# Kernel tuning notes

Hardware: AMD Instinct MI355X
Metric: run time of the kernel (lower is better)

Reference implementation:

```python
import jax, jax.numpy as jnp
import numpy as np

KS = 11  # conv kernel size, padding = KS//2 -> SAME


def setup_inputs() -> dict:
    key = jax.random.key(0)
    ks = jax.random.split(key, 6)
    B, H, W = 16, 256, 256
    x = jax.random.uniform(ks[0], (B, 1, H, W), jnp.float32)
    # conv_same(1,1,ks=11,bias=False) -> OIHW kernel [1,1,11,11]
    K = jax.random.normal(ks[1], (1, 1, KS, KS), jnp.float32) * (1.0 / KS)
    # rule: Linear(1,10) -> ReLU -> Linear(10,10) -> ReLU -> Linear(10,1), all with bias
    w1 = jax.random.normal(ks[2], (10, 1), jnp.float32) * 0.5
    b1 = jnp.zeros((10,), jnp.float32)
    w2 = jax.random.normal(ks[3], (10, 10), jnp.float32) * 0.3
    b2 = jnp.zeros((10,), jnp.float32)
    w3 = jax.random.normal(ks[4], (1, 10), jnp.float32) * 0.3
    b3 = jnp.zeros((1,), jnp.float32)
    return {"x": x, "K": K, "w1": w1, "b1": b1, "w2": w2, "b2": b2,
            "w3": w3, "b3": b3, "steps": 16}


def reference(x, K, w1, b1, w2, b2, w3, b3, steps):
    # One NCA step: 11x11 single-channel conv -> pointwise 3-layer MLP on the
    # channel dim (Permute makes Linear act per-pixel) -> clipped residual add.
    def step(xc, _):
        out = jax.lax.conv_general_dilated(
            xc, K, window_strides=(1, 1), padding="SAME",
            dimension_numbers=("NCHW", "OIHW", "NCHW"))  # [B,1,H,W]
        v = out[:, 0]                                   # [B,H,W]
        h = jax.nn.relu(v[..., None] * w1[:, 0] + b1)   # [B,H,W,10]
        h = jax.nn.relu(jnp.einsum("bhwi,oi->bhwo", h, w2) + b2)
        y = jnp.einsum("bhwi,oi->bhwo", h, w3) + b3     # [B,H,W,1]
        xn = jnp.clip(xc + jnp.moveaxis(y, -1, 1), 0.0, 1.0)
        return xn, xn

    _, seq = jax.lax.scan(step, x, None, length=steps)
    # torch returns a list [x0, x1, ..., x_steps]; we stack it.
    return jnp.concatenate([x[None], seq], axis=0)  # [steps+1, B, 1, H, W]
```

## Files before the change

### kernel.cpp

```cpp
#include <hip/hip_runtime.h>


#define HH 256
#define WW 256
#define BB 16
#define TH 16
#define TW 64
#define SH (TH + 10)
#define SW (TW + 10)
#define SWP 76
#define SLAB (BB * HH * WW)

__global__ __launch_bounds__(256) void nca_copy_x(const float* __restrict__ x,
                                                  float* __restrict__ out) {
    int i = (blockIdx.x * 256 + threadIdx.x) * 4;
    *(float4*)(out + i) = *(const float4*)(x + i);
}

__global__ __launch_bounds__(256) void nca_step(
    const float* __restrict__ src, float* __restrict__ dst,
    const float* __restrict__ Kk,
    const float* __restrict__ w1, const float* __restrict__ b1,
    const float* __restrict__ w2, const float* __restrict__ b2,
    const float* __restrict__ w3, const float* __restrict__ b3) {
    __shared__ __align__(16) float s[SH * SWP];

    const int tid = threadIdx.x;
    const int b   = blockIdx.z;
    const int gy0 = blockIdx.y * TH;
    const int gx0 = blockIdx.x * TW;
    const float* img = src + b * HH * WW;

    for (int i = tid; i < SH * SW; i += 256) {
        int r = i / SW, c = i - r * SW;
        int gy = gy0 - 5 + r, gx = gx0 - 5 + c;
        float v = 0.f;
        if (gy >= 0 && gy < HH && gx >= 0 && gx < WW) v = img[gy * WW + gx];
        s[r * SWP + c] = v;
    }
    __syncthreads();

    const int tx = tid & 15, ty = tid >> 4;
    const int x0 = tx * 4;

    float acc0 = 0.f, acc1 = 0.f, acc2 = 0.f, acc3 = 0.f;
#pragma unroll
    for (int ky = 0; ky < 11; ++ky) {
        const float* row = &s[(ty + ky) * SWP + x0];
        float win[16];
        *(float4*)(win + 0)  = *(const float4*)(row + 0);
        *(float4*)(win + 4)  = *(const float4*)(row + 4);
        *(float4*)(win + 8)  = *(const float4*)(row + 8);
        *(float2*)(win + 12) = *(const float2*)(row + 12);
#pragma unroll
        for (int kx = 0; kx < 11; ++kx) {
            float kv = Kk[ky * 11 + kx];
            acc0 = fmaf(win[kx + 0], kv, acc0);
            acc1 = fmaf(win[kx + 1], kv, acc1);
            acc2 = fmaf(win[kx + 2], kv, acc2);
            acc3 = fmaf(win[kx + 3], kv, acc3);
        }
    }

    const float b3v = b3[0];
    float vacc[4] = {acc0, acc1, acc2, acc3};
    float res[4];
#pragma unroll
    for (int p = 0; p < 4; ++p) {
        float v = vacc[p];
        float h1[10];
#pragma unroll
        for (int i = 0; i < 10; ++i)
            h1[i] = fmaxf(fmaf(v, w1[i], b1[i]), 0.f);
        float y = b3v;
#pragma unroll
        for (int o = 0; o < 10; ++o) {
            float a = b2[o];
#pragma unroll
            for (int i = 0; i < 10; ++i)
                a = fmaf(h1[i], w2[o * 10 + i], a);
            y = fmaf(fmaxf(a, 0.f), w3[o], y);
        }
        float xc = s[(ty + 5) * SWP + x0 + 5 + p];
        res[p] = fminf(fmaxf(xc + y, 0.f), 1.f);
    }

    float* orow = dst + b * HH * WW + (gy0 + ty) * WW + gx0 + x0;
    *(float4*)orow = make_float4(res[0], res[1], res[2], res[3]);
}

extern "C" void kernel_launch(void* const* d_in, const int* in_sizes, int n_in,
                              void* d_out, int out_size, void* d_ws, size_t ws_size,
                              hipStream_t stream) {
    const float* x  = (const float*)d_in[0];
    const float* Kk = (const float*)d_in[1];
    const float* w1 = (const float*)d_in[2];
    const float* b1 = (const float*)d_in[3];
    const float* w2 = (const float*)d_in[4];
    const float* b2 = (const float*)d_in[5];
    const float* w3 = (const float*)d_in[6];
    const float* b3 = (const float*)d_in[7];
    float* out = (float*)d_out;

    nca_copy_x<<<SLAB / (256 * 4), 256, 0, stream>>>(x, out);

    dim3 grid(WW / TW, HH / TH, BB);
    for (int k = 0; k < 16; ++k) {
        nca_step<<<grid, 256, 0, stream>>>(out + (size_t)k * SLAB,
                                           out + (size_t)(k + 1) * SLAB,
                                           Kk, w1, b1, w2, b2, w3, b3);
    }
}
```

Measured before the change: 288.4 us.

## Fuse all NCA steps into one persistent kernel with grid barriers

Replaces the copy kernel plus 16 per-step launches with a single persistent kernel of 1024 blocks that synchronises between steps through an atomic-counter grid barrier. The x0 copy is folded into the first step. Separately, when all b1 entries are zero, the first two MLP layers collapse into a per-sign linear map (relu(v*w1) = v*max(w1,0) for v>=0), so each pixel needs 10 FMAs for the hidden layer instead of about 110. The barrier depends on all 1024 blocks being co-resident, which is checked only through the occupancy query with no cooperative-launch guarantee. The fast MLP path relies on the test's zero biases but keeps a general fallback.

```diff
diff --git a/kernel.cpp b/kernel.cpp
--- a/kernel.cpp
+++ b/kernel.cpp
@@ -10,27 +10,51 @@
 #define SW (TW + 10)
 #define SWP 76
 #define SLAB (BB * HH * WW)
-
-__global__ __launch_bounds__(256) void nca_copy_x(const float* __restrict__ x,
-                                                  float* __restrict__ out) {
-    int i = (blockIdx.x * 256 + threadIdx.x) * 4;
-    *(float4*)(out + i) = *(const float4*)(x + i);
-}
-
-__global__ __launch_bounds__(256) void nca_step(
-    const float* __restrict__ src, float* __restrict__ dst,
+#define NSTEPS 16
+#define NB 1024
+
+__device__ __forceinline__ void grid_bar(unsigned* cnt, unsigned target) {
+    __syncthreads();
+    if (threadIdx.x == 0) {
+        __threadfence();
+        __hip_atomic_fetch_add(cnt, 1u, __ATOMIC_RELAXED, __HIP_MEMORY_SCOPE_AGENT);
+        while (__hip_atomic_load(cnt, __ATOMIC_RELAXED, __HIP_MEMORY_SCOPE_AGENT) < target)
+            __builtin_amdgcn_s_sleep(1);
+        __threadfence();
+    }
+    __syncthreads();
+}
+
+__device__ __forceinline__ void mlp_precompute(
+    const float* __restrict__ w1, const float* __restrict__ b1,
+    const float* __restrict__ w2, bool& fast, float (&cp)[10], float (&cn)[10]) {
+    fast = true;
+#pragma unroll
+    for (int i = 0; i < 10; ++i) fast = fast && (b1[i] == 0.f);
+#pragma unroll
+    for (int o = 0; o < 10; ++o) { cp[o] = 0.f; cn[o] = 0.f; }
+    if (fast) {
+#pragma unroll
+        for (int i = 0; i < 10; ++i) {
+            float wi = w1[i];
+            float p = fmaxf(wi, 0.f), n = fminf(wi, 0.f);
+#pragma unroll
+            for (int o = 0; o < 10; ++o) {
+                cp[o] = fmaf(p, w2[o * 10 + i], cp[o]);
+                cn[o] = fmaf(n, w2[o * 10 + i], cn[o]);
+            }
+        }
+    }
+}
+
+__device__ __forceinline__ void step_tile(
+    const float* __restrict__ img, float* __restrict__ dst, float* __restrict__ t0,
+    float* s, int gy0, int gx0, int tid, bool fast,
+    const float (&cp)[10], const float (&cn)[10],
     const float* __restrict__ Kk,
     const float* __restrict__ w1, const float* __restrict__ b1,
     const float* __restrict__ w2, const float* __restrict__ b2,
-    const float* __restrict__ w3, const float* __restrict__ b3) {
-    __shared__ __align__(16) float s[SH * SWP];
-
-    const int tid = threadIdx.x;
-    const int b   = blockIdx.z;
-    const int gy0 = blockIdx.y * TH;
-    const int gx0 = blockIdx.x * TW;
-    const float* img = src + b * HH * WW;
-
+    const float* __restrict__ w3, float b3v) {
     for (int i = tid; i < SH * SW; i += 256) {
         int r = i / SW, c = i - r * SW;
         int gy = gy0 - 5 + r, gx = gx0 - 5 + c;
@@ -62,31 +86,103 @@
         }
     }
 
-    const float b3v = b3[0];
     float vacc[4] = {acc0, acc1, acc2, acc3};
     float res[4];
-#pragma unroll
-    for (int p = 0; p < 4; ++p) {
-        float v = vacc[p];
-        float h1[10];
-#pragma unroll
-        for (int i = 0; i < 10; ++i)
-            h1[i] = fmaxf(fmaf(v, w1[i], b1[i]), 0.f);
-        float y = b3v;
-#pragma unroll
-        for (int o = 0; o < 10; ++o) {
-            float a = b2[o];
+    if (fast) {
+#pragma unroll
+        for (int p = 0; p < 4; ++p) {
+            float v = vacc[p];
+            bool pos = (v >= 0.f);
+            float y = b3v;
+#pragma unroll
+            for (int o = 0; o < 10; ++o) {
+                float c = pos ? cp[o] : cn[o];
+                float a = fmaf(v, c, b2[o]);
+                y = fmaf(fmaxf(a, 0.f), w3[o], y);
+            }
+            float xc = s[(ty + 5) * SWP + x0 + 5 + p];
+            res[p] = fminf(fmaxf(xc + y, 0.f), 1.f);
+        }
+    } else {
+#pragma unroll
+        for (int p = 0; p < 4; ++p) {
+            float v = vacc[p];
+            float h1[10];
 #pragma unroll
             for (int i = 0; i < 10; ++i)
-                a = fmaf(h1[i], w2[o * 10 + i], a);
-            y = fmaf(fmaxf(a, 0.f), w3[o], y);
-        }
-        float xc = s[(ty + 5) * SWP + x0 + 5 + p];
-        res[p] = fminf(fmaxf(xc + y, 0.f), 1.f);
-    }
-
-    float* orow = dst + b * HH * WW + (gy0 + ty) * WW + gx0 + x0;
+                h1[i] = fmaxf(fmaf(v, w1[i], b1[i]), 0.f);
+            float y = b3v;
+#pragma unroll
+            for (int o = 0; o < 10; ++o) {
+                float a = b2[o];
+#pragma unroll
+                for (int i = 0; i < 10; ++i)
+                    a = fmaf(h1[i], w2[o * 10 + i], a);
+                y = fmaf(fmaxf(a, 0.f), w3[o], y);
+            }
+            float xc = s[(ty + 5) * SWP + x0 + 5 + p];
+            res[p] = fminf(fmaxf(xc + y, 0.f), 1.f);
+        }
+    }
+
+    if (t0) {
+        const float* c0 = &s[(ty + 5) * SWP + x0 + 5];
+        float* o0 = t0 + (gy0 + ty) * WW + gx0 + x0;
+        *(float4*)o0 = make_float4(c0[0], c0[1], c0[2], c0[3]);
+    }
+    float* orow = dst + (gy0 + ty) * WW + gx0 + x0;
     *(float4*)orow = make_float4(res[0], res[1], res[2], res[3]);
+}
+
+__global__ __launch_bounds__(256, 4) void nca_persist(
+    const float* __restrict__ x, float* __restrict__ out, unsigned* cnt,
+    const float* __restrict__ Kk,
+    const float* __restrict__ w1, const float* __restrict__ b1,
+    const float* __restrict__ w2, const float* __restrict__ b2,
+    const float* __restrict__ w3, const float* __restrict__ b3) {
+    __shared__ __align__(16) float s[SH * SWP];
+    const int tid = threadIdx.x;
+    const int bid = blockIdx.x;
+    const int gx0 = (bid & 3) * TW;
+    const int gy0 = ((bid >> 2) & 15) * TH;
+    const int b   = bid >> 6;
+    const float b3v = b3[0];
+
+    bool fast; float cp[10], cn[10];
+    mlp_precompute(w1, b1, w2, fast, cp, cn);
+
+    for (int k = 0; k < NSTEPS; ++k) {
+        if (k > 0) grid_bar(cnt, (unsigned)(NB * k));
+        const float* img = (k == 0 ? x : out + (size_t)k * SLAB) + b * HH * WW;
+        float* dst = out + (size_t)(k + 1) * SLAB + b * HH * WW;
+        float* t0  = (k == 0) ? out + b * HH * WW : nullptr;
+        step_tile(img, dst, t0, s, gy0, gx0, tid, fast, cp, cn,
+                  Kk, w1, b1, w2, b2, w3, b3v);
+    }
+}
+
+__global__ __launch_bounds__(256) void nca_copy_x(const float* __restrict__ x,
+                                                  float* __restrict__ out) {
+    int i = (blockIdx.x * 256 + threadIdx.x) * 4;
+    *(float4*)(out + i) = *(const float4*)(x + i);
+}
+
+__global__ __launch_bounds__(256) void nca_step(
+    const float* __restrict__ src, float* __restrict__ dst,
+    const float* __restrict__ Kk,
+    const float* __restrict__ w1, const float* __restrict__ b1,
+    const float* __restrict__ w2, const float* __restrict__ b2,
+    const float* __restrict__ w3, const float* __restrict__ b3) {
+    __shared__ __align__(16) float s[SH * SWP];
+    const int tid = threadIdx.x;
+    const int b   = blockIdx.z;
+    const int gy0 = blockIdx.y * TH;
+    const int gx0 = blockIdx.x * TW;
+    const float b3v = b3[0];
+    bool fast; float cp[10], cn[10];
+    mlp_precompute(w1, b1, w2, fast, cp, cn);
+    step_tile(src + b * HH * WW, dst + b * HH * WW, nullptr, s, gy0, gx0, tid,
+              fast, cp, cn, Kk, w1, b1, w2, b2, w3, b3v);
 }
 
 extern "C" void kernel_launch(void* const* d_in, const int* in_sizes, int n_in,
@@ -102,12 +198,24 @@
     const float* b3 = (const float*)d_in[7];
     float* out = (float*)d_out;
 
-    nca_copy_x<<<SLAB / (256 * 4), 256, 0, stream>>>(x, out);
-
-    dim3 grid(WW / TW, HH / TH, BB);
-    for (int k = 0; k < 16; ++k) {
-        nca_step<<<grid, 256, 0, stream>>>(out + (size_t)k * SLAB,
-                                           out + (size_t)(k + 1) * SLAB,
-                                           Kk, w1, b1, w2, b2, w3, b3);
-    }
-}
+    static int maxb = -1;
+    if (maxb < 0) {
+        if (hipOccupancyMaxActiveBlocksPerMultiprocessor(
+                &maxb, (const void*)nca_persist, 256, 0) != hipSuccess)
+            maxb = 0;
+    }
+
+    if (maxb >= 4 && d_ws != nullptr && ws_size >= 64) {
+        hipMemsetAsync(d_ws, 0, 64, stream);
+        nca_persist<<<NB, 256, 0, stream>>>(x, out, (unsigned*)d_ws,
+                                            Kk, w1, b1, w2, b2, w3, b3);
+    } else {
+        nca_copy_x<<<SLAB / (256 * 4), 256, 0, stream>>>(x, out);
+        dim3 grid(WW / TW, HH / TH, BB);
+        for (int k = 0; k < 16; ++k) {
+            nca_step<<<grid, 256, 0, stream>>>(out + (size_t)k * SLAB,
+                                               out + (size_t)(k + 1) * SLAB,
+                                               Kk, w1, b1, w2, b2, w3, b3);
+        }
+    }
+}
```

Result: slower. 360.1 us (+24.8%).

## Collapse zero-bias MLP into sign-split linear form and fuse initial copy

Applied to the files above, without the earlier changes.

When the first-layer biases are all zero, relu(v*w1) is piecewise linear in v, so the first two layers fold into two precomputed 10-vectors chosen by the sign of v. This cuts the per-pixel MLP cost from about 110 FMAs to about 20. The separate kernel that copies x into output slot 0 is removed, and the first step writes that slab from its shared-memory tile. Each thread redoes a small per-block precompute, and a general fallback path remains for nonzero biases.

```diff
diff --git a/kernel.cpp b/kernel.cpp
--- a/kernel.cpp
+++ b/kernel.cpp
@@ -11,14 +11,60 @@
 #define SWP 76
 #define SLAB (BB * HH * WW)
 
-__global__ __launch_bounds__(256) void nca_copy_x(const float* __restrict__ x,
-                                                  float* __restrict__ out) {
-    int i = (blockIdx.x * 256 + threadIdx.x) * 4;
-    *(float4*)(out + i) = *(const float4*)(x + i);
+__device__ __forceinline__ void mlp_precompute(
+    const float* __restrict__ w1, const float* __restrict__ b1,
+    const float* __restrict__ w2, bool& fast, float (&cp)[10], float (&cn)[10]) {
+    fast = true;
+#pragma unroll
+    for (int i = 0; i < 10; ++i) fast = fast && (b1[i] == 0.f);
+#pragma unroll
+    for (int o = 0; o < 10; ++o) { cp[o] = 0.f; cn[o] = 0.f; }
+    if (fast) {
+#pragma unroll
+        for (int i = 0; i < 10; ++i) {
+            float wi = w1[i];
+            float p = fmaxf(wi, 0.f), n = fminf(wi, 0.f);
+#pragma unroll
+            for (int o = 0; o < 10; ++o) {
+                cp[o] = fmaf(p, w2[o * 10 + i], cp[o]);
+                cn[o] = fmaf(n, w2[o * 10 + i], cn[o]);
+            }
+        }
+    }
+}
+
+__device__ __forceinline__ float mlp_px(
+    float v, float xc, bool fast, const float (&cp)[10], const float (&cn)[10],
+    const float* __restrict__ w1, const float* __restrict__ b1,
+    const float* __restrict__ w2, const float* __restrict__ b2,
+    const float* __restrict__ w3, float b3v) {
+    float y = b3v;
+    if (fast) {
+        bool pos = (v >= 0.f);
+#pragma unroll
+        for (int o = 0; o < 10; ++o) {
+            float c = pos ? cp[o] : cn[o];
+            float a = fmaf(v, c, b2[o]);
+            y = fmaf(fmaxf(a, 0.f), w3[o], y);
+        }
+    } else {
+        float h1[10];
+#pragma unroll
+        for (int i = 0; i < 10; ++i) h1[i] = fmaxf(fmaf(v, w1[i], b1[i]), 0.f);
+#pragma unroll
+        for (int o = 0; o < 10; ++o) {
+            float a = b2[o];
+#pragma unroll
+            for (int i = 0; i < 10; ++i) a = fmaf(h1[i], w2[o * 10 + i], a);
+            y = fmaf(fmaxf(a, 0.f), w3[o], y);
+        }
+    }
+    return fminf(fmaxf(xc + y, 0.f), 1.f);
 }
 
 __global__ __launch_bounds__(256) void nca_step(
     const float* __restrict__ src, float* __restrict__ dst,
+    float* __restrict__ t0,
     const float* __restrict__ Kk,
     const float* __restrict__ w1, const float* __restrict__ b1,
     const float* __restrict__ w2, const float* __restrict__ b2,
@@ -30,6 +76,10 @@
     const int gy0 = blockIdx.y * TH;
     const int gx0 = blockIdx.x * TW;
     const float* img = src + b * HH * WW;
+    const float b3v = b3[0];
+
+    bool fast; float cp[10], cn[10];
+    mlp_precompute(w1, b1, w2, fast, cp, cn);
 
     for (int i = tid; i < SH * SW; i += 256) {
         int r = i / SW, c = i - r * SW;
@@ -42,6 +92,12 @@
 
     const int tx = tid & 15, ty = tid >> 4;
     const int x0 = tx * 4;
+
+    if (t0) {
+        const float* c0 = &s[(ty + 5) * SWP + x0 + 5];
+        float* o0 = t0 + b * HH * WW + (gy0 + ty) * WW + gx0 + x0;
+        *(float4*)o0 = make_float4(c0[0], c0[1], c0[2], c0[3]);
+    }
 
     float acc0 = 0.f, acc1 = 0.f, acc2 = 0.f, acc3 = 0.f;
 #pragma unroll
@@ -62,27 +118,12 @@
         }
     }
 
-    const float b3v = b3[0];
     float vacc[4] = {acc0, acc1, acc2, acc3};
     float res[4];
 #pragma unroll
     for (int p = 0; p < 4; ++p) {
-        float v = vacc[p];
-        float h1[10];
-#pragma unroll
-        for (int i = 0; i < 10; ++i)
-            h1[i] = fmaxf(fmaf(v, w1[i], b1[i]), 0.f);
-        float y = b3v;
-#pragma unroll
-        for (int o = 0; o < 10; ++o) {
-            float a = b2[o];
-#pragma unroll
-            for (int i = 0; i < 10; ++i)
-                a = fmaf(h1[i], w2[o * 10 + i], a);
-            y = fmaf(fmaxf(a, 0.f), w3[o], y);
-        }
         float xc = s[(ty + 5) * SWP + x0 + 5 + p];
-        res[p] = fminf(fmaxf(xc + y, 0.f), 1.f);
+        res[p] = mlp_px(vacc[p], xc, fast, cp, cn, w1, b1, w2, b2, w3, b3v);
     }
 
     float* orow = dst + b * HH * WW + (gy0 + ty) * WW + gx0 + x0;
@@ -102,12 +143,13 @@
     const float* b3 = (const float*)d_in[7];
     float* out = (float*)d_out;
 
-    nca_copy_x<<<SLAB / (256 * 4), 256, 0, stream>>>(x, out);
-
     dim3 grid(WW / TW, HH / TH, BB);
     for (int k = 0; k < 16; ++k) {
-        nca_step<<<grid, 256, 0, stream>>>(out + (size_t)k * SLAB,
-                                           out + (size_t)(k + 1) * SLAB,
-                                           Kk, w1, b1, w2, b2, w3, b3);
+        const float* src = (k == 0) ? x : out + (size_t)k * SLAB;
+        nca_step<<<grid, 256, 0, stream>>>(
+            src,
+            out + (size_t)(k + 1) * SLAB,
+            (k == 0) ? out : nullptr,
+            Kk, w1, b1, w2, b2, w3, b3);
     }
 }
```

After: 403.4 us. 1.4x slower.
